# Optimization experiments

Measured on AMD Instinct MI355X. Metric: run time of the kernel, lower is better.

## Reference

```python
import jax, jax.numpy as jnp
import numpy as np

D = 512      # dgm / hidden width
L = 3        # n_dgm_layers
B = 131072   # collocation batch
SCALE = 0.02 # init scale to keep gates unsaturated


def setup_inputs() -> dict:
    key = jax.random.key(0)
    ks = jax.random.split(key, 12)
    X = jax.random.normal(ks[0], (B, 2), jnp.float32)
    t = jax.random.uniform(ks[1], (B, 1), jnp.float32)
    # input layer: Linear(3, D)
    W_in = jax.random.normal(ks[2], (3, D), jnp.float32) * SCALE
    b_in = jnp.zeros((D,), jnp.float32)
    # dense hidden: Linear(D, D)
    W_h1 = jax.random.normal(ks[3], (D, D), jnp.float32) * SCALE
    b_h1 = jnp.zeros((D,), jnp.float32)
    # projection to dgm dims: Linear(D, D)
    W_hd = jax.random.normal(ks[4], (D, D), jnp.float32) * SCALE
    b_hd = jnp.zeros((D,), jnp.float32)
    # DGM layers: 12 linears each, order [Uz,Wz,Bz, Ug,Wg,Bg, Ur,Wr,Br, Uh,Wh,Bh]
    dgm_W = jax.random.normal(ks[5], (L, 12, D, D), jnp.float32) * SCALE
    dgm_b = jnp.zeros((L, 12, D), jnp.float32)
    # output head: Linear(D, 1)
    W_out = jax.random.normal(ks[6], (D, 1), jnp.float32) * SCALE
    b_out = jnp.zeros((1,), jnp.float32)
    return {"X": X, "t": t, "W_in": W_in, "b_in": b_in, "W_h1": W_h1,
            "b_h1": b_h1, "W_hd": W_hd, "b_hd": b_hd, "dgm_W": dgm_W,
            "dgm_b": dgm_b, "W_out": W_out, "b_out": b_out}


def reference(X, t, W_in, b_in, W_h1, b_h1, W_hd, b_hd, dgm_W, dgm_b, W_out, b_out):
    inp = jnp.concatenate([X, t], axis=1)          # [B, 3]
    x = jnp.tanh(inp @ W_in + b_in)                # input layer + tanh
    x = jnp.tanh(x @ W_h1 + b_h1)                  # hidden Linear + tanh
    x = x @ W_hd + b_hd                            # hidden -> dgm projection (no act)
    S1 = x
    S = x
    for l in range(L):                             # small fixed layer loop
        W = dgm_W[l]
        b = dgm_b[l]
        lin = lambda i, v: v @ W[i] + b[i]
        Z = jax.nn.sigmoid(lin(0, x) + lin(1, S) + lin(2, S1))
        G = jax.nn.sigmoid(lin(3, x) + lin(4, S1) + lin(5, S))
        R = jax.nn.sigmoid(lin(6, x) + lin(7, S) + lin(8, S1))
        H = jnp.tanh(lin(9, x) + lin(10, S * R) + lin(11, S1))
        S = (1.0 - G) * H + Z * S
    return S @ W_out + b_out                       # [B, 1]
```

## Files before the change

### kernel.cpp

```cpp
#include <hip/hip_runtime.h>
#include <stdint.h>

namespace {

constexpr int B_ROWS = 131072;

typedef __attribute__((ext_vector_type(8))) short bf16x8;
typedef __attribute__((ext_vector_type(4))) float f32x4;

__device__ __forceinline__ unsigned short f2bf(float f) {
  unsigned u = __builtin_bit_cast(unsigned, f);
  u += 0x7fffu + ((u >> 16) & 1u);
  return (unsigned short)(u >> 16);
}
__device__ __forceinline__ float bf2f(unsigned short h) {
  unsigned u = ((unsigned)h) << 16;
  return __builtin_bit_cast(float, u);
}
__device__ __forceinline__ float sigm(float v) { return 1.0f / (1.0f + __expf(-v)); }


__global__ void pack_t_k(const float* __restrict__ W, unsigned short* __restrict__ Wt) {
  int idx = blockIdx.x * 256 + threadIdx.x;
  int n = idx >> 9, k = idx & 511;
  Wt[idx] = f2bf(W[(k << 9) + n]);
}

__global__ void pack_zgr_k(const float* __restrict__ dgmW, unsigned short* __restrict__ Wt) {
  long idx = (long)blockIdx.x * 256 + threadIdx.x;
  int l = (int)(idx / (1536 * 1024));
  int rest = (int)(idx - (long)l * (1536 * 1024));
  int n = rest >> 10, k = rest & 1023;
  int g = n >> 9, nn = n & 511;
  const int xi0[3] = {0, 3, 6};
  const int xi1[3] = {2, 4, 8};
  const int si[3] = {1, 5, 7};
  float v;
  if (k < 512)
    v = dgmW[(((long)(l * 12 + xi0[g]) << 9) + k) * 512 + nn] +
        dgmW[(((long)(l * 12 + xi1[g]) << 9) + k) * 512 + nn];
  else
    v = dgmW[(((long)(l * 12 + si[g]) << 9) + (k - 512)) * 512 + nn];
  Wt[idx] = f2bf(v);
}

__global__ void pack_h_k(const float* __restrict__ dgmW, unsigned short* __restrict__ Wt) {
  long idx = (long)blockIdx.x * 256 + threadIdx.x;
  int l = (int)(idx / (512 * 1024));
  int rest = (int)(idx - (long)l * (512 * 1024));
  int n = rest >> 10, k = rest & 1023;
  float v;
  if (k < 512)
    v = dgmW[(((long)(l * 12 + 9) << 9) + k) * 512 + n] +
        dgmW[(((long)(l * 12 + 11) << 9) + k) * 512 + n];
  else
    v = dgmW[(((long)(l * 12 + 10) << 9) + (k - 512)) * 512 + n];
  Wt[idx] = f2bf(v);
}

__global__ void pack_bias_k(const float* __restrict__ dgmb, float* __restrict__ bzgr,
                            float* __restrict__ bh) {
  int idx = blockIdx.x * 256 + threadIdx.x;
  if (idx >= 3 * 2048) return;
  int l = idx >> 11, n = idx & 2047;
  const float* bl = dgmb + l * 12 * 512;
  if (n < 1536) {
    int g = n >> 9, nn = n & 511;
    bzgr[l * 1536 + n] =
        bl[(g * 3 + 0) * 512 + nn] + bl[(g * 3 + 1) * 512 + nn] + bl[(g * 3 + 2) * 512 + nn];
  } else {
    int nn = n - 1536;
    bh[l * 512 + nn] = bl[9 * 512 + nn] + bl[10 * 512 + nn] + bl[11 * 512 + nn];
  }
}

__global__ void front0_k(const float* __restrict__ X, const float* __restrict__ t,
                         const float* __restrict__ Win, const float* __restrict__ bin,
                         unsigned short* __restrict__ x0, long row0) {
  long idx = (long)blockIdx.x * 256 + threadIdx.x;
  long r = idx >> 9;
  int c = (int)(idx & 511);
  long gr = row0 + r;
  float a = X[gr * 2] * Win[c] + X[gr * 2 + 1] * Win[512 + c] + t[gr] * Win[1024 + c] + bin[c];
  x0[idx] = f2bf(tanhf(a));
}

__global__ void head_k(const unsigned short* __restrict__ S, const float* __restrict__ Wout,
                       const float* __restrict__ bout, float* __restrict__ out, long row0) {
  const int lane = threadIdx.x & 63, wid = threadIdx.x >> 6;
  const long r = (long)blockIdx.x * 4 + wid;
  bf16x8 sv = *(const bf16x8*)&S[r * 512 + lane * 8];
  float sum = 0.f;
#pragma unroll
  for (int i = 0; i < 8; ++i) sum += bf2f((unsigned short)sv[i]) * Wout[lane * 8 + i];
#pragma unroll
  for (int off = 32; off > 0; off >>= 1) sum += __shfl_down(sum, off);
  if (lane == 0) out[row0 + r] = sum + bout[0];
}

#define GLD(gsrc, ldst)                                                      \
  __builtin_amdgcn_global_load_lds(                                          \
      (const __attribute__((address_space(1))) void*)(gsrc),                 \
      (__attribute__((address_space(3))) void*)(ldst), 16, 0, 0)

template <int EPI, int KT>
__global__ __launch_bounds__(256, 4) void gemmS_k(
    const unsigned short* __restrict__ a0, const unsigned short* __restrict__ a1,
    const unsigned short* __restrict__ wt, const float* __restrict__ bias,
    unsigned short* __restrict__ o0, unsigned short* __restrict__ o1,
    unsigned short* __restrict__ o2, const unsigned short* __restrict__ e0,
    const unsigned short* __restrict__ e1) {
  constexpr int K = KT * 64;
  __shared__ unsigned short lds[12288];
  const int tid = threadIdx.x;
  const int lane = tid & 63, wid = tid >> 6;
  const int wm = wid >> 1, wn = wid & 1;
  const int lr = lane & 15, kk = lane >> 4;

  const int gx = gridDim.x;
  const int nwg = gx * (int)gridDim.y;
  const int orig = (int)blockIdx.y * gx + (int)blockIdx.x;
  const int q = nwg >> 3, rr = nwg & 7;
  const int xcd = orig & 7, lo = orig >> 3;
  const int wg = ((xcd < rr) ? xcd * (q + 1) : rr * (q + 1) + (xcd - rr) * q) + lo;
  const long brow = (long)(wg / gx) * 128;
  const int bcol = (wg % gx) * 64;

  const int gp8 = ((kk ^ ((lr >> 1) & 3)) << 3);
  const int a_rd = (wm * 64 + lr) * 32 + gp8;
  const int b_rd = 8192 + (wn * 32 + lr) * 32 + gp8;

  f32x4 acc[4][2] = {};

  auto stage = [&](int kt) {
    const unsigned short* src = (KT == 16 && (kt & 8)) ? a1 : a0;
    const int ko = (kt & 7) * 64;
#pragma unroll
    for (int i = 0; i < 4; ++i) {
      const int u = tid + (i << 8);
      const int ks = u >> 9, rem = u & 511;
      const int row = rem >> 2;
      const int gl = (rem & 3) ^ ((row >> 1) & 3);
      GLD(src + (brow + row) * 512 + ko + ks * 32 + gl * 8, lds + u * 8);
    }
#pragma unroll
    for (int i = 0; i < 2; ++i) {
      const int u = tid + (i << 8);
      const int ks = u >> 8, rem = u & 255;
      const int row = rem >> 2;
      const int gl = (rem & 3) ^ ((row >> 1) & 3);
      GLD(wt + (size_t)(bcol + row) * K + kt * 64 + ks * 32 + gl * 8, lds + 8192 + u * 8);
    }
  };

  for (int t = 0; t < KT; ++t) {
    __syncthreads();
    stage(t);
    __syncthreads();
#pragma unroll
    for (int ks = 0; ks < 2; ++ks) {
      bf16x8 bf0 = *(const bf16x8*)(lds + b_rd + ks * 2048);
      bf16x8 bf1 = *(const bf16x8*)(lds + b_rd + ks * 2048 + 512);
      bf16x8 af[4];
#pragma unroll
      for (int m = 0; m < 4; ++m)
        af[m] = *(const bf16x8*)(lds + a_rd + ks * 4096 + m * 512);
      __builtin_amdgcn_s_setprio(1);
#pragma unroll
      for (int m = 0; m < 4; ++m) {
        acc[m][0] = __builtin_amdgcn_mfma_f32_16x16x32_bf16(af[m], bf0, acc[m][0], 0, 0, 0);
        acc[m][1] = __builtin_amdgcn_mfma_f32_16x16x32_bf16(af[m], bf1, acc[m][1], 0, 0, 0);
      }
      __builtin_amdgcn_s_setprio(0);
    }
  }

#pragma unroll
  for (int m = 0; m < 4; ++m) {
#pragma unroll
    for (int n = 0; n < 2; ++n) {
      const int col = bcol + wn * 32 + n * 16 + lr;
      const float bs = bias[col];
#pragma unroll
      for (int j = 0; j < 4; ++j) {
        const long row = brow + wm * 64 + m * 16 + kk * 4 + j;
        float v = acc[m][n][j] + bs;
        if constexpr (EPI == 0) {
          o0[row * 512 + col] = f2bf(tanhf(v));
        } else if constexpr (EPI == 1) {
          unsigned short b = f2bf(v);
          o0[row * 512 + col] = b;
          o1[row * 512 + col] = b;
        } else if constexpr (EPI == 2) {
          const int g = col >> 9;
          const int nn = col & 511;
          const float sgv = sigm(v);
          if (g == 0) {
            o0[row * 512 + nn] = f2bf(sgv * bf2f(e0[row * 512 + nn]));
          } else if (g == 1) {
            o1[row * 512 + nn] = f2bf(1.0f - sgv);
          } else {
            o2[row * 512 + nn] = f2bf(sgv * bf2f(e0[row * 512 + nn]));
          }
        } else {
          const float h = tanhf(v);
          const float omg = bf2f(e0[row * 512 + col]);
          const float zs = bf2f(e1[row * 512 + col]);
          o0[row * 512 + col] = f2bf(omg * h + zs);
        }
      }
    }
  }
}

}

extern "C" void kernel_launch(void* const* d_in, const int* in_sizes, int n_in,
                              void* d_out, int out_size, void* d_ws, size_t ws_size,
                              hipStream_t stream) {
  const float* X = (const float*)d_in[0];
  const float* t = (const float*)d_in[1];
  const float* W_in = (const float*)d_in[2];
  const float* b_in = (const float*)d_in[3];
  const float* W_h1 = (const float*)d_in[4];
  const float* b_h1 = (const float*)d_in[5];
  const float* W_hd = (const float*)d_in[6];
  const float* b_hd = (const float*)d_in[7];
  const float* dgm_W = (const float*)d_in[8];
  const float* dgm_b = (const float*)d_in[9];
  const float* W_out = (const float*)d_in[10];
  const float* b_out = (const float*)d_in[11];
  float* out = (float*)d_out;
  char* ws = (char*)d_ws;

  size_t off = 0;
  auto alloc = [&](size_t bytes) {
    size_t o = off;
    off = (off + bytes + 255) & ~(size_t)255;
    return o;
  };
  size_t o_wth1 = alloc((size_t)512 * 512 * 2);
  size_t o_wthd = alloc((size_t)512 * 512 * 2);
  size_t o_wtzgr = alloc((size_t)3 * 1536 * 1024 * 2);
  size_t o_wth = alloc((size_t)3 * 512 * 1024 * 2);
  size_t o_bzgr = alloc((size_t)3 * 1536 * 4);
  size_t o_bh = alloc((size_t)3 * 512 * 4);
  size_t actoff = off;

  unsigned short* wth1 = (unsigned short*)(ws + o_wth1);
  unsigned short* wthd = (unsigned short*)(ws + o_wthd);
  unsigned short* wtzgr = (unsigned short*)(ws + o_wtzgr);
  unsigned short* wth = (unsigned short*)(ws + o_wth);
  float* bzgr = (float*)(ws + o_bzgr);
  float* bh = (float*)(ws + o_bh);

  size_t avail = ws_size > actoff ? ws_size - actoff : 0;
  int nch = 1;
  while (nch < 256 && (size_t)(B_ROWS / nch) * 512 * 2 * 5 > avail) nch <<= 1;
  const int R = B_ROWS / nch;
  unsigned short* xb = (unsigned short*)(ws + actoff);
  unsigned short* Sb = xb + (size_t)R * 512;
  unsigned short* ZSb = Sb + (size_t)R * 512;
  unsigned short* OGb = ZSb + (size_t)R * 512;
  unsigned short* SRb = OGb + (size_t)R * 512;

  pack_t_k<<<1024, 256, 0, stream>>>(W_h1, wth1);
  pack_t_k<<<1024, 256, 0, stream>>>(W_hd, wthd);
  pack_zgr_k<<<18432, 256, 0, stream>>>(dgm_W, wtzgr);
  pack_h_k<<<6144, 256, 0, stream>>>(dgm_W, wth);
  pack_bias_k<<<24, 256, 0, stream>>>(dgm_b, bzgr, bh);

  const int MT = R / 128;
  for (int c = 0; c < nch; ++c) {
    long row0 = (long)c * R;
    dim3 g8(8, MT), g24(24, MT);
    front0_k<<<R * 2, 256, 0, stream>>>(X, t, W_in, b_in, ZSb, row0);
    gemmS_k<0, 8><<<g8, 256, 0, stream>>>(ZSb, ZSb, wth1, b_h1, OGb, nullptr, nullptr,
                                          nullptr, nullptr);
    gemmS_k<1, 8><<<g8, 256, 0, stream>>>(OGb, OGb, wthd, b_hd, xb, Sb, nullptr,
                                          nullptr, nullptr);
    for (int l = 0; l < 3; ++l) {
      gemmS_k<2, 16><<<g24, 256, 0, stream>>>(xb, Sb, wtzgr + (size_t)l * 1536 * 1024,
                                              bzgr + l * 1536, ZSb, OGb, SRb, Sb, nullptr);
      gemmS_k<3, 16><<<g8, 256, 0, stream>>>(xb, SRb, wth + (size_t)l * 512 * 1024,
                                             bh + l * 512, Sb, nullptr, nullptr, OGb, ZSb);
    }
    head_k<<<R / 4, 256, 0, stream>>>(Sb, W_out, b_out, out, row0);
  }
}
```

Measured before the change: 3.013 ms.

## Double-buffer GEMM LDS stages with halved K-step and raise occupancy hint

Restructures the GEMM main loop so the K step shrinks from 64 to 32 and LDS holds two ping-pong buffers. The next tile's global-to-LDS load is issued before the current tile's MFMAs, and each iteration has one barrier instead of two. Launch bounds are raised to 6 waves-groups per CU to encourage higher occupancy. The cost is twice as many loop iterations with fewer MFMAs per barrier, plus possible register pressure from the tighter launch bound.

```diff
diff --git a/kernel.cpp b/kernel.cpp
--- a/kernel.cpp
+++ b/kernel.cpp
@@ -104,13 +104,13 @@
       (__attribute__((address_space(3))) void*)(ldst), 16, 0, 0)
 
 template <int EPI, int KT>
-__global__ __launch_bounds__(256, 4) void gemmS_k(
+__global__ __launch_bounds__(256, 6) void gemmS_k(
     const unsigned short* __restrict__ a0, const unsigned short* __restrict__ a1,
     const unsigned short* __restrict__ wt, const float* __restrict__ bias,
     unsigned short* __restrict__ o0, unsigned short* __restrict__ o1,
     unsigned short* __restrict__ o2, const unsigned short* __restrict__ e0,
     const unsigned short* __restrict__ e1) {
-  constexpr int K = KT * 64;
+  constexpr int K = KT * 32;
   __shared__ unsigned short lds[12288];
   const int tid = threadIdx.x;
   const int lane = tid & 63, wid = tid >> 6;
@@ -128,51 +128,47 @@
 
   const int gp8 = ((kk ^ ((lr >> 1) & 3)) << 3);
   const int a_rd = (wm * 64 + lr) * 32 + gp8;
-  const int b_rd = 8192 + (wn * 32 + lr) * 32 + gp8;
+  const int b_rd = 4096 + (wn * 32 + lr) * 32 + gp8;
 
   f32x4 acc[4][2] = {};
 
-  auto stage = [&](int kt) {
-    const unsigned short* src = (KT == 16 && (kt & 8)) ? a1 : a0;
-    const int ko = (kt & 7) * 64;
-#pragma unroll
-    for (int i = 0; i < 4; ++i) {
-      const int u = tid + (i << 8);
-      const int ks = u >> 9, rem = u & 511;
-      const int row = rem >> 2;
-      const int gl = (rem & 3) ^ ((row >> 1) & 3);
-      GLD(src + (brow + row) * 512 + ko + ks * 32 + gl * 8, lds + u * 8);
-    }
+  auto stage = [&](int kt, int dbo) {
+    const unsigned short* src = (KT == 32 && (kt & 16)) ? a1 : a0;
+    const int ko = (kt & 15) * 32;
 #pragma unroll
     for (int i = 0; i < 2; ++i) {
       const int u = tid + (i << 8);
-      const int ks = u >> 8, rem = u & 255;
-      const int row = rem >> 2;
-      const int gl = (rem & 3) ^ ((row >> 1) & 3);
-      GLD(wt + (size_t)(bcol + row) * K + kt * 64 + ks * 32 + gl * 8, lds + 8192 + u * 8);
+      const int row = u >> 2;
+      const int gl = (u & 3) ^ ((row >> 1) & 3);
+      GLD(src + (brow + row) * 512 + ko + gl * 8, lds + dbo + u * 8);
+    }
+    {
+      const int u = tid;
+      const int row = u >> 2;
+      const int gl = (u & 3) ^ ((row >> 1) & 3);
+      GLD(wt + (size_t)(bcol + row) * K + kt * 32 + gl * 8, lds + dbo + 4096 + u * 8);
     }
   };
 
+  stage(0, 0);
+  __syncthreads();
+
   for (int t = 0; t < KT; ++t) {
+    const int dbo = (t & 1) * 6144;
+    if (t + 1 < KT) stage(t + 1, dbo ^ 6144);
+    bf16x8 af[4];
+    bf16x8 bf0 = *(const bf16x8*)(lds + dbo + b_rd);
+    bf16x8 bf1 = *(const bf16x8*)(lds + dbo + b_rd + 512);
+#pragma unroll
+    for (int m = 0; m < 4; ++m) af[m] = *(const bf16x8*)(lds + dbo + a_rd + m * 512);
+    __builtin_amdgcn_s_setprio(1);
+#pragma unroll
+    for (int m = 0; m < 4; ++m) {
+      acc[m][0] = __builtin_amdgcn_mfma_f32_16x16x32_bf16(af[m], bf0, acc[m][0], 0, 0, 0);
+      acc[m][1] = __builtin_amdgcn_mfma_f32_16x16x32_bf16(af[m], bf1, acc[m][1], 0, 0, 0);
+    }
+    __builtin_amdgcn_s_setprio(0);
     __syncthreads();
-    stage(t);
-    __syncthreads();
-#pragma unroll
-    for (int ks = 0; ks < 2; ++ks) {
-      bf16x8 bf0 = *(const bf16x8*)(lds + b_rd + ks * 2048);
-      bf16x8 bf1 = *(const bf16x8*)(lds + b_rd + ks * 2048 + 512);
-      bf16x8 af[4];
-#pragma unroll
-      for (int m = 0; m < 4; ++m)
-        af[m] = *(const bf16x8*)(lds + a_rd + ks * 4096 + m * 512);
-      __builtin_amdgcn_s_setprio(1);
-#pragma unroll
-      for (int m = 0; m < 4; ++m) {
-        acc[m][0] = __builtin_amdgcn_mfma_f32_16x16x32_bf16(af[m], bf0, acc[m][0], 0, 0, 0);
-        acc[m][1] = __builtin_amdgcn_mfma_f32_16x16x32_bf16(af[m], bf1, acc[m][1], 0, 0, 0);
-      }
-      __builtin_amdgcn_s_setprio(0);
-    }
   }
 
 #pragma unroll
@@ -275,14 +271,14 @@
     long row0 = (long)c * R;
     dim3 g8(8, MT), g24(24, MT);
     front0_k<<<R * 2, 256, 0, stream>>>(X, t, W_in, b_in, ZSb, row0);
-    gemmS_k<0, 8><<<g8, 256, 0, stream>>>(ZSb, ZSb, wth1, b_h1, OGb, nullptr, nullptr,
-                                          nullptr, nullptr);
-    gemmS_k<1, 8><<<g8, 256, 0, stream>>>(OGb, OGb, wthd, b_hd, xb, Sb, nullptr,
-                                          nullptr, nullptr);
+    gemmS_k<0, 16><<<g8, 256, 0, stream>>>(ZSb, ZSb, wth1, b_h1, OGb, nullptr, nullptr,
+                                           nullptr, nullptr);
+    gemmS_k<1, 16><<<g8, 256, 0, stream>>>(OGb, OGb, wthd, b_hd, xb, Sb, nullptr,
+                                           nullptr, nullptr);
     for (int l = 0; l < 3; ++l) {
-      gemmS_k<2, 16><<<g24, 256, 0, stream>>>(xb, Sb, wtzgr + (size_t)l * 1536 * 1024,
+      gemmS_k<2, 32><<<g24, 256, 0, stream>>>(xb, Sb, wtzgr + (size_t)l * 1536 * 1024,
                                               bzgr + l * 1536, ZSb, OGb, SRb, Sb, nullptr);
-      gemmS_k<3, 16><<<g8, 256, 0, stream>>>(xb, SRb, wth + (size_t)l * 512 * 1024,
+      gemmS_k<3, 32><<<g8, 256, 0, stream>>>(xb, SRb, wth + (size_t)l * 512 * 1024,
                                              bh + l * 512, Sb, nullptr, nullptr, OGb, ZSb);
     }
     head_k<<<R / 4, 256, 0, stream>>>(Sb, W_out, b_out, out, row0);
```

Result: slower. 3.513 ms (+16.6%).

## Load B operand directly to registers and prefetch next K-tile during MFMA

Applied to the files above, without the earlier changes.

Weight (B) fragments are now read from global memory straight into registers instead of being staged through LDS, which shrinks the LDS buffer. The K loop is restructured as a software pipeline: A fragments are read from LDS, then the next tile's A (via LDS DMA) and B (into the alternate register set) are issued before the current tile's MFMAs run. The aim is to overlap global loads with compute and cut LDS usage and traffic. In exchange it uses more registers, makes uncoalesced per-lane global loads for B, and still has two barriers per tile.

```diff
diff --git a/kernel.cpp b/kernel.cpp
--- a/kernel.cpp
+++ b/kernel.cpp
@@ -111,7 +111,7 @@
     unsigned short* __restrict__ o2, const unsigned short* __restrict__ e0,
     const unsigned short* __restrict__ e1) {
   constexpr int K = KT * 64;
-  __shared__ unsigned short lds[12288];
+  __shared__ unsigned short lds[8192];
   const int tid = threadIdx.x;
   const int lane = tid & 63, wid = tid >> 6;
   const int wm = wid >> 1, wn = wid & 1;
@@ -128,9 +128,9 @@
 
   const int gp8 = ((kk ^ ((lr >> 1) & 3)) << 3);
   const int a_rd = (wm * 64 + lr) * 32 + gp8;
-  const int b_rd = 8192 + (wn * 32 + lr) * 32 + gp8;
 
   f32x4 acc[4][2] = {};
+  bf16x8 BA[4], BB[4];
 
   auto stage = [&](int kt) {
     const unsigned short* src = (KT == 16 && (kt & 8)) ? a1 : a0;
@@ -143,37 +143,54 @@
       const int gl = (rem & 3) ^ ((row >> 1) & 3);
       GLD(src + (brow + row) * 512 + ko + ks * 32 + gl * 8, lds + u * 8);
     }
-#pragma unroll
-    for (int i = 0; i < 2; ++i) {
-      const int u = tid + (i << 8);
-      const int ks = u >> 8, rem = u & 255;
-      const int row = rem >> 2;
-      const int gl = (rem & 3) ^ ((row >> 1) & 3);
-      GLD(wt + (size_t)(bcol + row) * K + kt * 64 + ks * 32 + gl * 8, lds + 8192 + u * 8);
-    }
   };
 
-  for (int t = 0; t < KT; ++t) {
-    __syncthreads();
-    stage(t);
-    __syncthreads();
-#pragma unroll
-    for (int ks = 0; ks < 2; ++ks) {
-      bf16x8 bf0 = *(const bf16x8*)(lds + b_rd + ks * 2048);
-      bf16x8 bf1 = *(const bf16x8*)(lds + b_rd + ks * 2048 + 512);
-      bf16x8 af[4];
-#pragma unroll
-      for (int m = 0; m < 4; ++m)
-        af[m] = *(const bf16x8*)(lds + a_rd + ks * 4096 + m * 512);
-      __builtin_amdgcn_s_setprio(1);
-#pragma unroll
-      for (int m = 0; m < 4; ++m) {
-        acc[m][0] = __builtin_amdgcn_mfma_f32_16x16x32_bf16(af[m], bf0, acc[m][0], 0, 0, 0);
-        acc[m][1] = __builtin_amdgcn_mfma_f32_16x16x32_bf16(af[m], bf1, acc[m][1], 0, 0, 0);
-      }
-      __builtin_amdgcn_s_setprio(0);
-    }
+  const size_t bln = (size_t)(bcol + wn * 32 + lr) * K + kk * 8;
+
+#define BFETCH(kt, dst)                                                       \
+  do {                                                                        \
+    _Pragma("unroll") for (int _n = 0; _n < 2; ++_n) _Pragma("unroll") for (  \
+        int _ks = 0; _ks < 2; ++_ks) dst[_n * 2 + _ks] =                      \
+        *(const bf16x8*)(wt + bln + (size_t)_n * 16 * K + (kt)*64 + _ks * 32);\
+  } while (0)
+
+#define TILE_BODY(t, Bc, Bn)                                                  \
+  do {                                                                        \
+    bf16x8 af0[4], af1[4];                                                    \
+    _Pragma("unroll") for (int _m = 0; _m < 4; ++_m) af0[_m] =                \
+        *(const bf16x8*)(lds + a_rd + _m * 512);                              \
+    _Pragma("unroll") for (int _m = 0; _m < 4; ++_m) af1[_m] =                \
+        *(const bf16x8*)(lds + a_rd + 4096 + _m * 512);                       \
+    __syncthreads();           \
+    if ((t) + 1 < KT) {                                                       \
+      stage((t) + 1);                                                         \
+      BFETCH((t) + 1, Bn);                                                    \
+    }                                                                         \
+    _Pragma("unroll") for (int _m = 0; _m < 4; ++_m) {                        \
+      acc[_m][0] =                                                            \
+          __builtin_amdgcn_mfma_f32_16x16x32_bf16(af0[_m], Bc[0], acc[_m][0], 0, 0, 0); \
+      acc[_m][1] =                                                            \
+          __builtin_amdgcn_mfma_f32_16x16x32_bf16(af0[_m], Bc[2], acc[_m][1], 0, 0, 0); \
+    }                                                                         \
+    _Pragma("unroll") for (int _m = 0; _m < 4; ++_m) {                        \
+      acc[_m][0] =                                                            \
+          __builtin_amdgcn_mfma_f32_16x16x32_bf16(af1[_m], Bc[1], acc[_m][0], 0, 0, 0); \
+      acc[_m][1] =                                                            \
+          __builtin_amdgcn_mfma_f32_16x16x32_bf16(af1[_m], Bc[3], acc[_m][1], 0, 0, 0); \
+    }                                                                         \
+    __syncthreads();       \
+  } while (0)
+
+  BFETCH(0, BA);
+  stage(0);
+  __syncthreads();
+
+  for (int t = 0; t < KT; t += 2) {
+    TILE_BODY(t, BA, BB);
+    TILE_BODY(t + 1, BB, BA);
   }
+#undef TILE_BODY
+#undef BFETCH
 
 #pragma unroll
   for (int m = 0; m < 4; ++m) {
```

Measured after the change: 4.942 ms. +64.0%, slower.
